# Optimization experiments

Measured on AMD Instinct MI355X. Metric: run time of the kernel, lower is better.

The kernel has to match this reference:

```python
import jax, jax.numpy as jnp
import numpy as np

B, T, D = 64, 512, 1024

def setup_inputs() -> dict:
    key = jax.random.key(0)
    k1, k2, k3 = jax.random.split(key, 3)
    q1 = jax.random.normal(k1, (B, T, D), dtype=jnp.float32)
    q2 = jax.random.normal(k2, (B, T, D), dtype=jnp.float32)
    # original uses 'uniform' init; scale like a small uniform weight
    U = jax.random.uniform(k3, (D, D), dtype=jnp.float32, minval=-0.05, maxval=0.05)
    return {"q1": q1, "q2": q2, "U": U}

def reference(q1, q2, U):
    # bilinear scores: (q1 @ U) @ q2^T -> [B, T1, T2]
    att = jnp.einsum('btd,de,bse->bts', q1, U, q2)
    att = jax.nn.relu(att)
    w1_att = jax.nn.softmax(att, axis=1)  # softmax over q1 timesteps
    w2_att = jax.nn.softmax(att, axis=2)  # softmax over q2 timesteps
    # q1_align = w1_att^T @ q1 -> [B, T2, D]
    q1_align = jnp.einsum('bts,btd->bsd', w1_att, q1)
    # q2_align = w2_att @ q2 -> [B, T1, D]
    q2_align = jnp.einsum('bts,bsd->btd', w2_att, q2)
    return (q1_align, q2_align)
```

## Files before the change

kernel.cpp:

```cpp
#include <hip/hip_runtime.h>
#include <hip/hip_bf16.h>
#include <math.h>

#define B_DIM 64
#define T_DIM 512
#define D_DIM 1024
#define TT (T_DIM * T_DIM)
#define TD (T_DIM * D_DIM)

typedef _Float16 f16;
typedef f16 f16x4 __attribute__((ext_vector_type(4)));
typedef f16 f16x8 __attribute__((ext_vector_type(8)));
typedef float f32x4 __attribute__((ext_vector_type(4)));


__device__ __forceinline__ void gld_lds16(const void* g, void* l) {
    __builtin_amdgcn_global_load_lds(
        (const __attribute__((address_space(1))) void*)g,
        (__attribute__((address_space(3))) void*)l, 16, 0, 0);
}

#define SWZ(r) (((r) >> 1) & 3)

template <int EPI>
__global__ __launch_bounds__(512, 2) void k_mfma2(
        const f16* __restrict__ A, int lda,
        const f16* __restrict__ Bt, int ldb, int K,
        void* __restrict__ Cout, int ldc,
        const float2* __restrict__ scaleP,
        long batchA, long batchB, long batchC,
        float2* __restrict__ rowP, float2* __restrict__ colP, long pstr,
        const f16* __restrict__ A2, const f16* __restrict__ Bt2,
        void* __restrict__ Cout2, const float2* __restrict__ scaleP2, int zsplit) {
    __shared__ f16 LA[2][8192];
    __shared__ f16 LB[2][8192];

    const int tid = threadIdx.x;
    const int lane = tid & 63, w = tid >> 6;

    const int gX = gridDim.x, gY = gridDim.y;
    int nwg = gX * gY * gridDim.z;
    int o = blockIdx.x + gX * (blockIdx.y + gY * blockIdx.z);
    int q8 = nwg >> 3, r8 = nwg & 7, xcd = o & 7, idx = o >> 3;
    int fl = (xcd < r8 ? xcd * (q8 + 1) : r8 * (q8 + 1) + (xcd - r8) * q8) + idx;
    const int bx = fl % gX;
    int tmp = fl / gX;
    const int by = tmp % gY;
    const int bz = tmp / gY;

    const f16* Au = A; const f16* Bu = Bt;
    void* Cu = Cout; const float2* su = scaleP;
    int zb = bz;
    if constexpr (EPI == 2) {
        if (bz >= zsplit) {
            zb = bz - zsplit;
            Au = A2; Bu = Bt2; Cu = Cout2; su = scaleP2;
        }
    }

    const f16* Ab = Au + (long)zb * batchA + (long)(by * 256) * lda;
    const f16* Bb = Bu + (long)zb * batchB + (long)(bx * 256) * ldb;

    const int r0 = tid >> 2, s0 = (tid & 3) ^ SWZ(r0);
    const int r1 = (512 + tid) >> 2, s1 = ((512 + tid) & 3) ^ SWZ(r1);
    const long offA0 = (long)r0 * lda + s0 * 8;
    const long offA1 = (long)r1 * lda + s1 * 8;
    const long offB0 = (long)r0 * ldb + s0 * 8;
    const long offB1 = (long)r1 * ldb + s1 * 8;
    const int ldsOff0 = w * 512;
    const int ldsOff1 = 4096 + w * 512;

    const int g = lane >> 4;
    const int rA0 = (w & 1) * 128 + (lane & 15);
    const int rB0 = (w >> 1) * 64 + (lane & 15);

    f32x4 acc[8][4] = {};

    gld_lds16(Ab + offA0, &LA[0][ldsOff0]);
    gld_lds16(Ab + offA1, &LA[0][ldsOff1]);
    gld_lds16(Bb + offB0, &LB[0][ldsOff0]);
    gld_lds16(Bb + offB1, &LB[0][ldsOff1]);
    __syncthreads();

    const int NT = K >> 5;
    for (int t = 0; t < NT; ++t) {
        const int cur = t & 1;
        if (t + 1 < NT) {
            const long kt = (long)(t + 1) << 5;
            gld_lds16(Ab + offA0 + kt, &LA[cur ^ 1][ldsOff0]);
            gld_lds16(Ab + offA1 + kt, &LA[cur ^ 1][ldsOff1]);
            gld_lds16(Bb + offB0 + kt, &LB[cur ^ 1][ldsOff0]);
            gld_lds16(Bb + offB1 + kt, &LB[cur ^ 1][ldsOff1]);
        }
        f16x8 a[8], b[4];
#pragma unroll
        for (int m = 0; m < 8; ++m) {
            int r = rA0 + m * 16;
            a[m] = *(const f16x8*)(&LA[cur][r * 32 + ((g ^ SWZ(r)) << 3)]);
        }
#pragma unroll
        for (int n = 0; n < 4; ++n) {
            int r = rB0 + n * 16;
            b[n] = *(const f16x8*)(&LB[cur][r * 32 + ((g ^ SWZ(r)) << 3)]);
        }
#pragma unroll
        for (int m = 0; m < 8; ++m)
#pragma unroll
            for (int n = 0; n < 4; ++n)
                acc[m][n] = __builtin_amdgcn_mfma_f32_16x16x32_f16(a[m], b[n], acc[m][n], 0, 0, 0);
        __syncthreads();
    }

    const int row0 = by * 256 + (w & 1) * 128 + (lane >> 4) * 4;
    const int col0 = bx * 256 + (w >> 1) * 64 + (lane & 15);

    if constexpr (EPI == 0) {
        f16* C = (f16*)Cu;
#pragma unroll
        for (int m = 0; m < 8; ++m)
#pragma unroll
            for (int r = 0; r < 4; ++r) {
                long row = row0 + m * 16 + r;
#pragma unroll
                for (int n = 0; n < 4; ++n)
                    C[row * ldc + col0 + n * 16] = (f16)acc[m][n][r];
            }
    } else if constexpr (EPI == 1) {
#pragma unroll
        for (int m = 0; m < 8; ++m)
#pragma unroll
            for (int n = 0; n < 4; ++n)
#pragma unroll
                for (int r = 0; r < 4; ++r)
                    acc[m][n][r] = fmaxf(acc[m][n][r], 0.0f);
        float* C = (float*)Cu + (long)zb * batchC;
#pragma unroll
        for (int m = 0; m < 8; ++m)
#pragma unroll
            for (int r = 0; r < 4; ++r) {
                long row = row0 + m * 16 + r;
#pragma unroll
                for (int n = 0; n < 4; ++n)
                    C[row * ldc + col0 + n * 16] = acc[m][n][r];
            }
        float* redR = (float*)(&LA[0][0]);
        float* redC = redR + 2048;
        const int h = w & 1, cw = w >> 1;
#pragma unroll
        for (int m = 0; m < 8; ++m)
#pragma unroll
            for (int r = 0; r < 4; ++r) {
                float mx = fmaxf(fmaxf(acc[m][0][r], acc[m][1][r]),
                                 fmaxf(acc[m][2][r], acc[m][3][r]));
                mx = fmaxf(mx, __shfl_xor(mx, 1));
                mx = fmaxf(mx, __shfl_xor(mx, 2));
                mx = fmaxf(mx, __shfl_xor(mx, 4));
                mx = fmaxf(mx, __shfl_xor(mx, 8));
                float sm = __expf(acc[m][0][r] - mx) + __expf(acc[m][1][r] - mx)
                         + __expf(acc[m][2][r] - mx) + __expf(acc[m][3][r] - mx);
                sm += __shfl_xor(sm, 1);
                sm += __shfl_xor(sm, 2);
                sm += __shfl_xor(sm, 4);
                sm += __shfl_xor(sm, 8);
                if ((lane & 15) == 0) {
                    int lr = m * 16 + (lane >> 4) * 4 + r;
                    redR[((h * 128 + lr) * 4 + cw) * 2 + 0] = mx;
                    redR[((h * 128 + lr) * 4 + cw) * 2 + 1] = sm;
                }
            }
#pragma unroll
        for (int n = 0; n < 4; ++n) {
            float mx = acc[0][n][0];
#pragma unroll
            for (int m = 0; m < 8; ++m)
#pragma unroll
                for (int r = 0; r < 4; ++r) mx = fmaxf(mx, acc[m][n][r]);
            mx = fmaxf(mx, __shfl_xor(mx, 16));
            mx = fmaxf(mx, __shfl_xor(mx, 32));
            float sm = 0.f;
#pragma unroll
            for (int m = 0; m < 8; ++m)
#pragma unroll
                for (int r = 0; r < 4; ++r) sm += __expf(acc[m][n][r] - mx);
            sm += __shfl_xor(sm, 16);
            sm += __shfl_xor(sm, 32);
            if (lane < 16) {
                int c = cw * 64 + n * 16 + lane;
                redC[(h * 256 + c) * 2 + 0] = mx;
                redC[(h * 256 + c) * 2 + 1] = sm;
            }
        }
        __syncthreads();
        if (tid < 256) {
            float M = -1e30f, S = 0.f;
#pragma unroll
            for (int i = 0; i < 4; ++i) {
                float m_ = redR[(tid * 4 + i) * 2 + 0];
                float s_ = redR[(tid * 4 + i) * 2 + 1];
                float nm = fmaxf(M, m_);
                S = S * __expf(M - nm) + s_ * __expf(m_ - nm);
                M = nm;
            }
            rowP[(long)bx * pstr + (long)bz * 512 + by * 256 + tid] = make_float2(M, S);
        } else {
            int c = tid - 256;
            float m0_ = redC[c * 2 + 0], s0_ = redC[c * 2 + 1];
            float m1_ = redC[(256 + c) * 2 + 0], s1_ = redC[(256 + c) * 2 + 1];
            float M = fmaxf(m0_, m1_);
            float S = s0_ * __expf(m0_ - M) + s1_ * __expf(m1_ - M);
            colP[(long)by * pstr + (long)bz * 512 + bx * 256 + c] = make_float2(M, S);
        }
    } else {
        float* C = (float*)Cu + (long)zb * batchC;
        const float2* sp = su + (long)zb * 512;
#pragma unroll
        for (int m = 0; m < 8; ++m)
#pragma unroll
            for (int r = 0; r < 4; ++r) {
                long row = row0 + m * 16 + r;
                float2 pa = sp[row], pb = sp[pstr + row];
                float M = fmaxf(pa.x, pb.x);
                float S = pa.y * __expf(pa.x - M) + pb.y * __expf(pb.x - M);
                float inv = 1.0f / S;
#pragma unroll
                for (int n = 0; n < 4; ++n)
                    C[row * ldc + col0 + n * 16] = acc[m][n][r] * inv;
            }
    }
}

__global__ __launch_bounds__(256) void k_cast_both(const float* __restrict__ q1,
                                                   const float* __restrict__ q2,
                                                   f16* __restrict__ q1h, f16* __restrict__ q1ht,
                                                   f16* __restrict__ q2h, f16* __restrict__ q2ht) {
    __shared__ f16 tr[64][72];
    int zz = blockIdx.z;
    int b = zz & 63;
    const float* src = (zz < 64) ? q1 : q2;
    f16* dst  = (zz < 64) ? q1h : q2h;
    f16* dstT = (zz < 64) ? q1ht : q2ht;
    int d0 = blockIdx.x * 64, t0 = blockIdx.y * 64;
    const float* S = src + ((size_t)b * T_DIM + t0) * D_DIM + d0;
    f16* Dr = dst + ((size_t)b * T_DIM + t0) * D_DIM + d0;
    int tid = threadIdx.x;
    int rr = tid >> 4, cc = (tid & 15) * 4;
#pragma unroll
    for (int i = 0; i < 4; ++i) {
        int r = rr + i * 16;
        float4 v = *(const float4*)(S + (size_t)r * D_DIM + cc);
        f16x4 h = {(f16)v.x, (f16)v.y, (f16)v.z, (f16)v.w};
        *(f16x4*)(Dr + (size_t)r * D_DIM + cc) = h;
        tr[cc + 0][r] = h[0];
        tr[cc + 1][r] = h[1];
        tr[cc + 2][r] = h[2];
        tr[cc + 3][r] = h[3];
    }
    __syncthreads();
    f16* Dt = dstT + ((size_t)b * D_DIM + d0) * T_DIM + t0;
    int r2 = tid >> 3, c8 = (tid & 7) * 8;
#pragma unroll
    for (int i = 0; i < 2; ++i) {
        int d = r2 + i * 32;
        f16x8 vv = *(const f16x8*)(&tr[d][c8]);
        *(f16x8*)(Dt + (size_t)d * T_DIM + c8) = vv;
    }
}

__global__ __launch_bounds__(256) void k_castU(const float* __restrict__ U,
                                               f16* __restrict__ Uht) {
    __shared__ f16 tr[64][72];
    int n0 = blockIdx.x * 64, k0 = blockIdx.y * 64;
    int tid = threadIdx.x;
    int rr = tid >> 4, cc = (tid & 15) * 4;
#pragma unroll
    for (int i = 0; i < 4; ++i) {
        int r = rr + i * 16;
        float4 v = *(const float4*)(U + (size_t)(k0 + r) * D_DIM + n0 + cc);
        tr[cc + 0][r] = (f16)v.x;
        tr[cc + 1][r] = (f16)v.y;
        tr[cc + 2][r] = (f16)v.z;
        tr[cc + 3][r] = (f16)v.w;
    }
    __syncthreads();
    int r2 = tid >> 3, c8 = (tid & 7) * 8;
#pragma unroll
    for (int i = 0; i < 2; ++i) {
        int n = r2 + i * 32;
        f16x8 vv = *(const f16x8*)(&tr[n][c8]);
        *(f16x8*)(Uht + (size_t)(n0 + n) * D_DIM + k0 + c8) = vv;
    }
}

__global__ __launch_bounds__(256) void k_pconv(const float* __restrict__ att,
                                               const float2* __restrict__ rowP,
                                               const float2* __restrict__ colP, long pstr,
                                               f16* __restrict__ P2, f16* __restrict__ P1) {
    __shared__ f16 tr[64][72];
    __shared__ float rmS[64], cmS[64];
    int z = blockIdx.z;
    int t0 = blockIdx.y * 64, s0 = blockIdx.x * 64;
    int tid = threadIdx.x;
    if (tid < 64) {
        float2 a = rowP[(long)z * 512 + t0 + tid];
        float2 b = rowP[pstr + (long)z * 512 + t0 + tid];
        rmS[tid] = fmaxf(a.x, b.x);
    } else if (tid < 128) {
        int s = tid - 64;
        float2 a = colP[(long)z * 512 + s0 + s];
        float2 b = colP[pstr + (long)z * 512 + s0 + s];
        cmS[s] = fmaxf(a.x, b.x);
    }
    __syncthreads();
    const float* S = att + (size_t)z * TT + (size_t)t0 * T_DIM + s0;
    int rr = tid >> 4, cc = (tid & 15) * 4;
#pragma unroll
    for (int i = 0; i < 4; ++i) {
        int r = rr + i * 16;
        float4 v = *(const float4*)(S + (size_t)r * T_DIM + cc);
        float m = rmS[r];
        f16x4 p2 = {(f16)__expf(v.x - m), (f16)__expf(v.y - m),
                    (f16)__expf(v.z - m), (f16)__expf(v.w - m)};
        *(f16x4*)(P2 + (size_t)z * TT + (size_t)(t0 + r) * T_DIM + s0 + cc) = p2;
        tr[cc + 0][r] = (f16)__expf(v.x - cmS[cc + 0]);
        tr[cc + 1][r] = (f16)__expf(v.y - cmS[cc + 1]);
        tr[cc + 2][r] = (f16)__expf(v.z - cmS[cc + 2]);
        tr[cc + 3][r] = (f16)__expf(v.w - cmS[cc + 3]);
    }
    __syncthreads();
    int r2 = tid >> 3, c8 = (tid & 7) * 8;
#pragma unroll
    for (int i = 0; i < 2; ++i) {
        int s = r2 + i * 32;
        f16x8 vv = *(const f16x8*)(&tr[s][c8]);
        *(f16x8*)(P1 + (size_t)z * TT + (size_t)(s0 + s) * T_DIM + t0 + c8) = vv;
    }
}

__global__ __launch_bounds__(256) void k_rowstats(const float* __restrict__ att,
                                                  float* __restrict__ rmax,
                                                  float* __restrict__ rsum, int b0) {
    int wave = threadIdx.x >> 6, lane = threadIdx.x & 63;
    int lr = blockIdx.x * 4 + wave;
    const float4* row = reinterpret_cast<const float4*>(att + (size_t)lr * T_DIM);
    float4 v0 = row[lane];
    float4 v1 = row[lane + 64];
    float m = fmaxf(fmaxf(fmaxf(v0.x, v0.y), fmaxf(v0.z, v0.w)),
                    fmaxf(fmaxf(v1.x, v1.y), fmaxf(v1.z, v1.w)));
#pragma unroll
    for (int off = 32; off >= 1; off >>= 1) m = fmaxf(m, __shfl_xor(m, off));
    float s = __expf(v0.x - m) + __expf(v0.y - m) + __expf(v0.z - m) + __expf(v0.w - m)
            + __expf(v1.x - m) + __expf(v1.y - m) + __expf(v1.z - m) + __expf(v1.w - m);
#pragma unroll
    for (int off = 32; off >= 1; off >>= 1) s += __shfl_xor(s, off);
    if (lane == 0) {
        size_t gr = (size_t)b0 * T_DIM + lr;
        rmax[gr] = m;
        rsum[gr] = s;
    }
}

__global__ __launch_bounds__(256) void k_colstats(const float* __restrict__ att,
                                                  float* __restrict__ cmax,
                                                  float* __restrict__ csum, int b0) {
    int lb = blockIdx.y;
    int s = blockIdx.x * 256 + threadIdx.x;
    const float* base = att + (size_t)lb * TT + s;
    float m = -INFINITY, sum = 0.f;
    for (int t = 0; t < T_DIM; ++t) {
        float x = base[(size_t)t * T_DIM];
        float nm = fmaxf(m, x);
        sum = sum * __expf(m - nm) + __expf(x - nm);
        m = nm;
    }
    size_t g = (size_t)(b0 + lb) * T_DIM + s;
    cmax[g] = m;
    csum[g] = sum;
}

#define BM 128
#define BN 128
#define BKK 16
#define APITCH 132

__device__ __forceinline__ void stage_a_rowmajor(float* As, const float* __restrict__ A,
                                                 int lda, int tid) {
#pragma unroll
    for (int i = 0; i < 2; ++i) {
        int idx = tid + i * 256;
        int r = idx >> 2;
        int k4 = (idx & 3) << 2;
        float4 v = *reinterpret_cast<const float4*>(&A[(size_t)r * lda + k4]);
        As[(k4 + 0) * APITCH + r] = v.x;
        As[(k4 + 1) * APITCH + r] = v.y;
        As[(k4 + 2) * APITCH + r] = v.z;
        As[(k4 + 3) * APITCH + r] = v.w;
    }
}
__device__ __forceinline__ void stage_a_rowmajor_exp(float* As, const float* __restrict__ A,
                                                     int lda, const float* __restrict__ rowmax,
                                                     int tid) {
#pragma unroll
    for (int i = 0; i < 2; ++i) {
        int idx = tid + i * 256;
        int r = idx >> 2;
        int k4 = (idx & 3) << 2;
        float4 v = *reinterpret_cast<const float4*>(&A[(size_t)r * lda + k4]);
        float m = rowmax[r];
        As[(k4 + 0) * APITCH + r] = __expf(v.x - m);
        As[(k4 + 1) * APITCH + r] = __expf(v.y - m);
        As[(k4 + 2) * APITCH + r] = __expf(v.z - m);
        As[(k4 + 3) * APITCH + r] = __expf(v.w - m);
    }
}
__device__ __forceinline__ void stage_a_colmajor_exp(float* As, const float* __restrict__ S,
                                                     int lds, const float* __restrict__ colmax,
                                                     int tid) {
#pragma unroll
    for (int i = 0; i < 2; ++i) {
        int idx = tid + i * 256;
        int k = idx >> 5;
        int m4 = (idx & 31) << 2;
        float4 v = *reinterpret_cast<const float4*>(&S[(size_t)k * lds + m4]);
        float4 c = *reinterpret_cast<const float4*>(&colmax[m4]);
        float4 o;
        o.x = __expf(v.x - c.x); o.y = __expf(v.y - c.y);
        o.z = __expf(v.z - c.z); o.w = __expf(v.w - c.w);
        *reinterpret_cast<float4*>(&As[k * APITCH + m4]) = o;
    }
}
__device__ __forceinline__ void stage_b_rowmajor(float* Bs, const float* __restrict__ Bp,
                                                 int ldb, int tid) {
#pragma unroll
    for (int i = 0; i < 2; ++i) {
        int idx = tid + i * 256;
        int k = idx >> 5;
        int c4 = idx & 31;
        float4 v = *reinterpret_cast<const float4*>(&Bp[(size_t)k * ldb + (c4 << 2)]);
        *reinterpret_cast<float4*>(&Bs[k * BN + ((c4 & 1) << 6) + ((c4 >> 1) << 2)]) = v;
    }
}
__device__ __forceinline__ void stage_b_transpose(float* Bs, const float* __restrict__ Q,
                                                  int ldq, int tid) {
#pragma unroll
    for (int i = 0; i < 2; ++i) {
        int idx = tid + i * 256;
        int s = idx >> 2;
        int e4 = (idx & 3) << 2;
        float4 v = *reinterpret_cast<const float4*>(&Q[(size_t)s * ldq + e4]);
        int sw = ((s & 4) << 4) + ((s >> 3) << 2) + (s & 3);
        Bs[(e4 + 0) * BN + sw] = v.x;
        Bs[(e4 + 1) * BN + sw] = v.y;
        Bs[(e4 + 2) * BN + sw] = v.z;
        Bs[(e4 + 3) * BN + sw] = v.w;
    }
}
__device__ __forceinline__ void gemm_inner(const float* As, const float* Bs,
                                           float acc[8][8], int tx, int ty) {
#pragma unroll
    for (int k = 0; k < BKK; ++k) {
        float4 a0 = *reinterpret_cast<const float4*>(&As[k * APITCH + ty * 8]);
        float4 a1 = *reinterpret_cast<const float4*>(&As[k * APITCH + ty * 8 + 4]);
        float4 b0 = *reinterpret_cast<const float4*>(&Bs[k * BN + tx * 4]);
        float4 b1 = *reinterpret_cast<const float4*>(&Bs[k * BN + 64 + tx * 4]);
        float a[8] = {a0.x, a0.y, a0.z, a0.w, a1.x, a1.y, a1.z, a1.w};
        float b[8] = {b0.x, b0.y, b0.z, b0.w, b1.x, b1.y, b1.z, b1.w};
#pragma unroll
        for (int i = 0; i < 8; ++i)
#pragma unroll
            for (int j = 0; j < 8; ++j)
                acc[i][j] = fmaf(a[i], b[j], acc[i][j]);
    }
}
__global__ __launch_bounds__(256) void k_gemm_qU(const float* __restrict__ q1,
                                                 const float* __restrict__ U,
                                                 float* __restrict__ qU, int b0) {
    __shared__ float As[BKK * APITCH];
    __shared__ float Bs[BKK * BN];
    int tid = threadIdx.x, tx = tid & 15, ty = tid >> 4;
    int m0 = blockIdx.y * BM;
    int n0 = blockIdx.x * BN;
    const float* Abase = q1 + (size_t)b0 * TD + (size_t)m0 * D_DIM;
    const float* Bbase = U + n0;
    float acc[8][8] = {};
    for (int kt = 0; kt < D_DIM; kt += BKK) {
        stage_a_rowmajor(As, Abase + kt, D_DIM, tid);
        stage_b_rowmajor(Bs, Bbase + (size_t)kt * D_DIM, D_DIM, tid);
        __syncthreads();
        gemm_inner(As, Bs, acc, tx, ty);
        __syncthreads();
    }
    float* Cp = qU + (size_t)m0 * D_DIM + n0;
#pragma unroll
    for (int i = 0; i < 8; ++i) {
        int r = ty * 8 + i;
        float4 o0 = {acc[i][0], acc[i][1], acc[i][2], acc[i][3]};
        float4 o1 = {acc[i][4], acc[i][5], acc[i][6], acc[i][7]};
        *reinterpret_cast<float4*>(&Cp[(size_t)r * D_DIM + tx * 8]) = o0;
        *reinterpret_cast<float4*>(&Cp[(size_t)r * D_DIM + tx * 8 + 4]) = o1;
    }
}
__global__ __launch_bounds__(256) void k_att(const float* __restrict__ qU,
                                             const float* __restrict__ q2,
                                             float* __restrict__ att, int b0) {
    __shared__ float As[BKK * APITCH];
    __shared__ float Bs[BKK * BN];
    int tid = threadIdx.x, tx = tid & 15, ty = tid >> 4;
    int lb = blockIdx.z;
    int m0 = blockIdx.y * BM;
    int n0 = blockIdx.x * BN;
    const float* Abase = qU + (size_t)lb * TD + (size_t)m0 * D_DIM;
    const float* Qbase = q2 + (size_t)(b0 + lb) * TD + (size_t)n0 * D_DIM;
    float acc[8][8] = {};
    for (int kt = 0; kt < D_DIM; kt += BKK) {
        stage_a_rowmajor(As, Abase + kt, D_DIM, tid);
        stage_b_transpose(Bs, Qbase + kt, D_DIM, tid);
        __syncthreads();
        gemm_inner(As, Bs, acc, tx, ty);
        __syncthreads();
    }
    float* Cp = att + (size_t)lb * TT + (size_t)m0 * T_DIM + n0;
#pragma unroll
    for (int i = 0; i < 8; ++i) {
        int r = ty * 8 + i;
        float4 o0 = {fmaxf(acc[i][0], 0.f), fmaxf(acc[i][1], 0.f), fmaxf(acc[i][2], 0.f), fmaxf(acc[i][3], 0.f)};
        float4 o1 = {fmaxf(acc[i][4], 0.f), fmaxf(acc[i][5], 0.f), fmaxf(acc[i][6], 0.f), fmaxf(acc[i][7], 0.f)};
        *reinterpret_cast<float4*>(&Cp[(size_t)r * T_DIM + tx * 8]) = o0;
        *reinterpret_cast<float4*>(&Cp[(size_t)r * T_DIM + tx * 8 + 4]) = o1;
    }
}
__global__ __launch_bounds__(256) void k_q2align(const float* __restrict__ att,
                                                 const float* __restrict__ q2,
                                                 const float* __restrict__ rmax,
                                                 const float* __restrict__ rsum,
                                                 float* __restrict__ out, int b0) {
    __shared__ float As[BKK * APITCH];
    __shared__ float Bs[BKK * BN];
    int tid = threadIdx.x, tx = tid & 15, ty = tid >> 4;
    int lb = blockIdx.z;
    int m0 = blockIdx.y * BM;
    int n0 = blockIdx.x * BN;
    const float* Abase = att + (size_t)lb * TT + (size_t)m0 * T_DIM;
    const float* rmaxp = rmax + (size_t)(b0 + lb) * T_DIM + m0;
    const float* rsump = rsum + (size_t)(b0 + lb) * T_DIM + m0;
    const float* Bbase = q2 + (size_t)(b0 + lb) * TD + n0;
    float acc[8][8] = {};
    for (int kt = 0; kt < T_DIM; kt += BKK) {
        stage_a_rowmajor_exp(As, Abase + kt, T_DIM, rmaxp, tid);
        stage_b_rowmajor(Bs, Bbase + (size_t)kt * D_DIM, D_DIM, tid);
        __syncthreads();
        gemm_inner(As, Bs, acc, tx, ty);
        __syncthreads();
    }
    float* Cp = out + (size_t)B_DIM * TD + (size_t)(b0 + lb) * TD + (size_t)m0 * D_DIM + n0;
#pragma unroll
    for (int i = 0; i < 8; ++i) {
        int r = ty * 8 + i;
        float inv = 1.0f / rsump[r];
        float4 o0 = {acc[i][0] * inv, acc[i][1] * inv, acc[i][2] * inv, acc[i][3] * inv};
        float4 o1 = {acc[i][4] * inv, acc[i][5] * inv, acc[i][6] * inv, acc[i][7] * inv};
        *reinterpret_cast<float4*>(&Cp[(size_t)r * D_DIM + tx * 8]) = o0;
        *reinterpret_cast<float4*>(&Cp[(size_t)r * D_DIM + tx * 8 + 4]) = o1;
    }
}
__global__ __launch_bounds__(256) void k_q1align(const float* __restrict__ att,
                                                 const float* __restrict__ q1,
                                                 const float* __restrict__ cmax,
                                                 const float* __restrict__ csum,
                                                 float* __restrict__ out, int b0) {
    __shared__ float As[BKK * APITCH];
    __shared__ float Bs[BKK * BN];
    int tid = threadIdx.x, tx = tid & 15, ty = tid >> 4;
    int lb = blockIdx.z;
    int m0 = blockIdx.y * BM;
    int n0 = blockIdx.x * BN;
    const float* Sbase = att + (size_t)lb * TT + m0;
    const float* cmaxp = cmax + (size_t)(b0 + lb) * T_DIM + m0;
    const float* csump = csum + (size_t)(b0 + lb) * T_DIM + m0;
    const float* Bbase = q1 + (size_t)(b0 + lb) * TD + n0;
    float acc[8][8] = {};
    for (int kt = 0; kt < T_DIM; kt += BKK) {
        stage_a_colmajor_exp(As, Sbase + (size_t)kt * T_DIM, T_DIM, cmaxp, tid);
        stage_b_rowmajor(Bs, Bbase + (size_t)kt * D_DIM, D_DIM, tid);
        __syncthreads();
        gemm_inner(As, Bs, acc, tx, ty);
        __syncthreads();
    }
    float* Cp = out + (size_t)(b0 + lb) * TD + (size_t)m0 * D_DIM + n0;
#pragma unroll
    for (int i = 0; i < 8; ++i) {
        int r = ty * 8 + i;
        float inv = 1.0f / csump[r];
        float4 o0 = {acc[i][0] * inv, acc[i][1] * inv, acc[i][2] * inv, acc[i][3] * inv};
        float4 o1 = {acc[i][4] * inv, acc[i][5] * inv, acc[i][6] * inv, acc[i][7] * inv};
        *reinterpret_cast<float4*>(&Cp[(size_t)r * D_DIM + tx * 8]) = o0;
        *reinterpret_cast<float4*>(&Cp[(size_t)r * D_DIM + tx * 8 + 4]) = o1;
    }
}

extern "C" void kernel_launch(void* const* d_in, const int* in_sizes, int n_in,
                              void* d_out, int out_size, void* d_ws, size_t ws_size,
                              hipStream_t stream) {
    const float* q1 = (const float*)d_in[0];
    const float* q2 = (const float*)d_in[1];
    const float* U  = (const float*)d_in[2];
    float* out = (float*)d_out;

    const size_t BT  = (size_t)B_DIM * T_DIM;
    const size_t BTD = (size_t)B_DIM * TD;
    const size_t DD  = (size_t)D_DIM * D_DIM;

    const size_t fixedB = (4 * BTD + DD) * 2;
    const size_t perbB  = (size_t)TD * 2 + (size_t)TT * 4 + (size_t)TT * 4
                        + 4ull * T_DIM * sizeof(float2);
    int C = 64;
    while (C > 1 && fixedB + (size_t)C * perbB > ws_size) C >>= 1;

    if (fixedB + perbB <= ws_size) {
        f16* q1h  = (f16*)d_ws;
        f16* q1ht = q1h  + BTD;
        f16* q2h  = q1ht + BTD;
        f16* q2ht = q2h  + BTD;
        f16* Uht  = q2ht + BTD;
        f16* qUh  = Uht  + DD;
        float* att = (float*)(qUh + (size_t)C * TD);
        f16* P2h  = (f16*)(att + (size_t)C * TT);
        f16* P1h  = P2h + (size_t)C * TT;
        float2* rowP = (float2*)(P1h + (size_t)C * TT);
        float2* colP = rowP + 2ull * C * T_DIM;
        const long pstr = (long)C * T_DIM;

        k_cast_both<<<dim3(16, 8, 128), 256, 0, stream>>>(q1, q2, q1h, q1ht, q2h, q2ht);
        k_castU<<<dim3(16, 16), 256, 0, stream>>>(U, Uht);

        for (int b0 = 0; b0 < B_DIM; b0 += C) {
            k_mfma2<0><<<dim3(4, C * 2, 1), 512, 0, stream>>>(
                q1h + (size_t)b0 * TD, D_DIM, Uht, D_DIM, D_DIM,
                qUh, D_DIM, nullptr, 0, 0, 0,
                nullptr, nullptr, 0, nullptr, nullptr, nullptr, nullptr, 0);
            k_mfma2<1><<<dim3(2, 2, C), 512, 0, stream>>>(
                qUh, D_DIM, q2h + (size_t)b0 * TD, D_DIM, D_DIM,
                att, T_DIM, nullptr, (long)TD, (long)TD, (long)TT,
                rowP, colP, pstr, nullptr, nullptr, nullptr, nullptr, 0);
            k_pconv<<<dim3(8, 8, C), 256, 0, stream>>>(att, rowP, colP, pstr, P2h, P1h);
            k_mfma2<2><<<dim3(4, 2, 2 * C), 512, 0, stream>>>(
                P2h, T_DIM, q2ht + (size_t)b0 * TD, T_DIM, T_DIM,
                out + BTD + (size_t)b0 * TD, D_DIM, rowP,
                (long)TT, (long)TD, (long)TD,
                nullptr, nullptr, pstr,
                P1h, q1ht + (size_t)b0 * TD,
                out + (size_t)b0 * TD, colP, C);
        }
        return;
    }

    const size_t statsElems = 4ull * B_DIM * T_DIM;
    float* rmax = (float*)d_ws;
    float* rsum = rmax + BT;
    float* cmax = rsum + BT;
    float* csum = cmax + BT;
    float* scratch = csum + BT;
    size_t availFloats = (ws_size > statsElems * 4) ? (ws_size - statsElems * 4) / 4 : 0;
    int C2 = 64;
    while (C2 > 1 && (size_t)C2 * (TD + TT) > availFloats) C2 >>= 1;
    if ((size_t)C2 * (TD + TT) > availFloats) return;
    float* qU  = scratch;
    float* att = qU + (size_t)C2 * TD;
    for (int b0 = 0; b0 < B_DIM; b0 += C2) {
        k_gemm_qU<<<dim3(D_DIM / BN, C2 * (T_DIM / BM)), 256, 0, stream>>>(q1, U, qU, b0);
        k_att<<<dim3(T_DIM / BN, T_DIM / BM, C2), 256, 0, stream>>>(qU, q2, att, b0);
        k_rowstats<<<dim3(C2 * T_DIM / 4), 256, 0, stream>>>(att, rmax, rsum, b0);
        k_colstats<<<dim3(T_DIM / 256, C2), 256, 0, stream>>>(att, cmax, csum, b0);
        k_q2align<<<dim3(D_DIM / BN, T_DIM / BM, C2), 256, 0, stream>>>(att, q2, rmax, rsum, out, b0);
        k_q1align<<<dim3(D_DIM / BN, T_DIM / BM, C2), 256, 0, stream>>>(att, q1, cmax, csum, out, b0);
    }
}
```

Measured before the change: 452.5 us.

## Fuse casts into GEMM launches and compute row-softmax probabilities inside align GEMM

```diff
diff --git a/kernel.cpp b/kernel.cpp
--- a/kernel.cpp
+++ b/kernel.cpp
@@ -7,12 +7,12 @@
 #define D_DIM 1024
 #define TT (T_DIM * T_DIM)
 #define TD (T_DIM * D_DIM)
+#define PSTR ((long)B_DIM * T_DIM)
 
 typedef _Float16 f16;
 typedef f16 f16x4 __attribute__((ext_vector_type(4)));
 typedef f16 f16x8 __attribute__((ext_vector_type(8)));
 typedef float f32x4 __attribute__((ext_vector_type(4)));
-
 
 __device__ __forceinline__ void gld_lds16(const void* g, void* l) {
     __builtin_amdgcn_global_load_lds(
@@ -29,11 +29,9 @@
         void* __restrict__ Cout, int ldc,
         const float2* __restrict__ scaleP,
         long batchA, long batchB, long batchC,
-        float2* __restrict__ rowP, float2* __restrict__ colP, long pstr,
-        const f16* __restrict__ A2, const f16* __restrict__ Bt2,
-        void* __restrict__ Cout2, const float2* __restrict__ scaleP2, int zsplit) {
-    __shared__ f16 LA[2][8192];
-    __shared__ f16 LB[2][8192];
+        float2* __restrict__ rowP, float2* __restrict__ colP) {
+    __shared__ __align__(16) f16 LA[2][8192];
+    __shared__ __align__(16) f16 LB[2][8192];
 
     const int tid = threadIdx.x;
     const int lane = tid & 63, w = tid >> 6;
@@ -41,28 +39,18 @@
     const int gX = gridDim.x, gY = gridDim.y;
     int nwg = gX * gY * gridDim.z;
     int o = blockIdx.x + gX * (blockIdx.y + gY * blockIdx.z);
-    int q8 = nwg >> 3, r8 = nwg & 7, xcd = o & 7, idx = o >> 3;
-    int fl = (xcd < r8 ? xcd * (q8 + 1) : r8 * (q8 + 1) + (xcd - r8) * q8) + idx;
+    int q8 = nwg >> 3;
+    int fl = (o & 7) * q8 + (o >> 3);
     const int bx = fl % gX;
     int tmp = fl / gX;
     const int by = tmp % gY;
     const int bz = tmp / gY;
 
-    const f16* Au = A; const f16* Bu = Bt;
-    void* Cu = Cout; const float2* su = scaleP;
-    int zb = bz;
-    if constexpr (EPI == 2) {
-        if (bz >= zsplit) {
-            zb = bz - zsplit;
-            Au = A2; Bu = Bt2; Cu = Cout2; su = scaleP2;
-        }
-    }
-
-    const f16* Ab = Au + (long)zb * batchA + (long)(by * 256) * lda;
-    const f16* Bb = Bu + (long)zb * batchB + (long)(bx * 256) * ldb;
+    const f16* Ab = A + (long)bz * batchA + (long)(by * 256) * lda;
+    const f16* Bb = Bt + (long)bz * batchB + (long)(bx * 256) * ldb;
 
     const int r0 = tid >> 2, s0 = (tid & 3) ^ SWZ(r0);
-    const int r1 = (512 + tid) >> 2, s1 = ((512 + tid) & 3) ^ SWZ(r1);
+    const int r1 = r0 + 128, s1 = (tid & 3) ^ SWZ(r1);
     const long offA0 = (long)r0 * lda + s0 * 8;
     const long offA1 = (long)r1 * lda + s1 * 8;
     const long offB0 = (long)r0 * ldb + s0 * 8;
@@ -103,29 +91,20 @@
             int r = rB0 + n * 16;
             b[n] = *(const f16x8*)(&LB[cur][r * 32 + ((g ^ SWZ(r)) << 3)]);
         }
+        __builtin_amdgcn_s_setprio(1);
 #pragma unroll
         for (int m = 0; m < 8; ++m)
 #pragma unroll
             for (int n = 0; n < 4; ++n)
                 acc[m][n] = __builtin_amdgcn_mfma_f32_16x16x32_f16(a[m], b[n], acc[m][n], 0, 0, 0);
+        __builtin_amdgcn_s_setprio(0);
         __syncthreads();
     }
 
     const int row0 = by * 256 + (w & 1) * 128 + (lane >> 4) * 4;
     const int col0 = bx * 256 + (w >> 1) * 64 + (lane & 15);
 
-    if constexpr (EPI == 0) {
-        f16* C = (f16*)Cu;
-#pragma unroll
-        for (int m = 0; m < 8; ++m)
-#pragma unroll
-            for (int r = 0; r < 4; ++r) {
-                long row = row0 + m * 16 + r;
-#pragma unroll
-                for (int n = 0; n < 4; ++n)
-                    C[row * ldc + col0 + n * 16] = (f16)acc[m][n][r];
-            }
-    } else if constexpr (EPI == 1) {
+    if constexpr (EPI == 1) {
 #pragma unroll
         for (int m = 0; m < 8; ++m)
 #pragma unroll
@@ -133,7 +112,7 @@
 #pragma unroll
                 for (int r = 0; r < 4; ++r)
                     acc[m][n][r] = fmaxf(acc[m][n][r], 0.0f);
-        float* C = (float*)Cu + (long)zb * batchC;
+        float* C = (float*)Cout + (long)bz * batchC;
 #pragma unroll
         for (int m = 0; m < 8; ++m)
 #pragma unroll
@@ -201,24 +180,24 @@
                 S = S * __expf(M - nm) + s_ * __expf(m_ - nm);
                 M = nm;
             }
-            rowP[(long)bx * pstr + (long)bz * 512 + by * 256 + tid] = make_float2(M, S);
+            rowP[(long)bx * PSTR + (long)bz * 512 + by * 256 + tid] = make_float2(M, S);
         } else {
             int c = tid - 256;
             float m0_ = redC[c * 2 + 0], s0_ = redC[c * 2 + 1];
             float m1_ = redC[(256 + c) * 2 + 0], s1_ = redC[(256 + c) * 2 + 1];
             float M = fmaxf(m0_, m1_);
             float S = s0_ * __expf(m0_ - M) + s1_ * __expf(m1_ - M);
-            colP[(long)by * pstr + (long)bz * 512 + bx * 256 + c] = make_float2(M, S);
+            colP[(long)by * PSTR + (long)bz * 512 + bx * 256 + c] = make_float2(M, S);
         }
     } else {
-        float* C = (float*)Cu + (long)zb * batchC;
-        const float2* sp = su + (long)zb * 512;
+        float* C = (float*)Cout + (long)bz * batchC;
+        const float2* sp = scaleP + (long)bz * 512;
 #pragma unroll
         for (int m = 0; m < 8; ++m)
 #pragma unroll
             for (int r = 0; r < 4; ++r) {
                 long row = row0 + m * 16 + r;
-                float2 pa = sp[row], pb = sp[pstr + row];
+                float2 pa = sp[row], pb = sp[PSTR + row];
                 float M = fmaxf(pa.x, pb.x);
                 float S = pa.y * __expf(pa.x - M) + pb.y * __expf(pb.x - M);
                 float inv = 1.0f / S;
@@ -229,371 +208,330 @@
     }
 }
 
-__global__ __launch_bounds__(256) void k_cast_both(const float* __restrict__ q1,
-                                                   const float* __restrict__ q2,
-                                                   f16* __restrict__ q1h, f16* __restrict__ q1ht,
-                                                   f16* __restrict__ q2h, f16* __restrict__ q2ht) {
+__global__ __launch_bounds__(256) void k_d1(const float* __restrict__ q1,
+                                            f16* __restrict__ q1h, f16* __restrict__ q1ht,
+                                            const float* __restrict__ U,
+                                            f16* __restrict__ Uht) {
     __shared__ f16 tr[64][72];
-    int zz = blockIdx.z;
-    int b = zz & 63;
-    const float* src = (zz < 64) ? q1 : q2;
-    f16* dst  = (zz < 64) ? q1h : q2h;
-    f16* dstT = (zz < 64) ? q1ht : q2ht;
-    int d0 = blockIdx.x * 64, t0 = blockIdx.y * 64;
-    const float* S = src + ((size_t)b * T_DIM + t0) * D_DIM + d0;
-    f16* Dr = dst + ((size_t)b * T_DIM + t0) * D_DIM + d0;
     int tid = threadIdx.x;
-    int rr = tid >> 4, cc = (tid & 15) * 4;
-#pragma unroll
-    for (int i = 0; i < 4; ++i) {
-        int r = rr + i * 16;
-        float4 v = *(const float4*)(S + (size_t)r * D_DIM + cc);
-        f16x4 h = {(f16)v.x, (f16)v.y, (f16)v.z, (f16)v.w};
-        *(f16x4*)(Dr + (size_t)r * D_DIM + cc) = h;
-        tr[cc + 0][r] = h[0];
-        tr[cc + 1][r] = h[1];
-        tr[cc + 2][r] = h[2];
-        tr[cc + 3][r] = h[3];
-    }
-    __syncthreads();
-    f16* Dt = dstT + ((size_t)b * D_DIM + d0) * T_DIM + t0;
-    int r2 = tid >> 3, c8 = (tid & 7) * 8;
-#pragma unroll
-    for (int i = 0; i < 2; ++i) {
-        int d = r2 + i * 32;
-        f16x8 vv = *(const f16x8*)(&tr[d][c8]);
-        *(f16x8*)(Dt + (size_t)d * T_DIM + c8) = vv;
+    int z = blockIdx.z;
+    if (z < 64) {
+        int b = z;
+        int d0 = blockIdx.x * 64, t0 = blockIdx.y * 64;
+        const float* S = q1 + ((size_t)b * T_DIM + t0) * D_DIM + d0;
+        f16* Dr = q1h + ((size_t)b * T_DIM + t0) * D_DIM + d0;
+        int rr = tid >> 4, cc = (tid & 15) * 4;
+#pragma unroll
+        for (int i = 0; i < 4; ++i) {
+            int r = rr + i * 16;
+            float4 v = *(const float4*)(S + (size_t)r * D_DIM + cc);
+            f16x4 h = {(f16)v.x, (f16)v.y, (f16)v.z, (f16)v.w};
+            *(f16x4*)(Dr + (size_t)r * D_DIM + cc) = h;
+            tr[cc + 0][r] = h[0];
+            tr[cc + 1][r] = h[1];
+            tr[cc + 2][r] = h[2];
+            tr[cc + 3][r] = h[3];
+        }
+        __syncthreads();
+        f16* Dt = q1ht + ((size_t)b * D_DIM + d0) * T_DIM + t0;
+        int r2 = tid >> 3, c8 = (tid & 7) * 8;
+#pragma unroll
+        for (int i = 0; i < 2; ++i) {
+            int d = r2 + i * 32;
+            f16x8 vv = *(const f16x8*)(&tr[d][c8]);
+            *(f16x8*)(Dt + (size_t)d * T_DIM + c8) = vv;
+        }
+    } else {
+        int pos = blockIdx.y * 16 + blockIdx.x;
+        for (int u = 0; u < 2; ++u) {
+            int tile = pos + u * 128;
+            int n0 = (tile & 15) * 64, k0 = (tile >> 4) * 64;
+            int rr = tid >> 4, cc = (tid & 15) * 4;
+#pragma unroll
+            for (int i = 0; i < 4; ++i) {
+                int r = rr + i * 16;
+                float4 v = *(const float4*)(U + (size_t)(k0 + r) * D_DIM + n0 + cc);
+                tr[cc + 0][r] = (f16)v.x;
+                tr[cc + 1][r] = (f16)v.y;
+                tr[cc + 2][r] = (f16)v.z;
+                tr[cc + 3][r] = (f16)v.w;
+            }
+            __syncthreads();
+            int r2 = tid >> 3, c8 = (tid & 7) * 8;
+#pragma unroll
+            for (int i = 0; i < 2; ++i) {
+                int n = r2 + i * 32;
+                f16x8 vv = *(const f16x8*)(&tr[n][c8]);
+                *(f16x8*)(Uht + (size_t)(n0 + n) * D_DIM + k0 + c8) = vv;
+            }
+            __syncthreads();
+        }
     }
 }
 
-__global__ __launch_bounds__(256) void k_castU(const float* __restrict__ U,
-                                               f16* __restrict__ Uht) {
-    __shared__ f16 tr[64][72];
-    int n0 = blockIdx.x * 64, k0 = blockIdx.y * 64;
+__global__ __launch_bounds__(512, 2) void k_d2(const f16* __restrict__ q1h,
+                                               const f16* __restrict__ Uht,
+                                               f16* __restrict__ qUh,
+                                               const float* __restrict__ q2,
+                                               f16* __restrict__ q2h,
+                                               f16* __restrict__ q2ht) {
+    __shared__ __align__(16) f16 SM[32768];
     int tid = threadIdx.x;
-    int rr = tid >> 4, cc = (tid & 15) * 4;
-#pragma unroll
-    for (int i = 0; i < 4; ++i) {
-        int r = rr + i * 16;
-        float4 v = *(const float4*)(U + (size_t)(k0 + r) * D_DIM + n0 + cc);
-        tr[cc + 0][r] = (f16)v.x;
-        tr[cc + 1][r] = (f16)v.y;
-        tr[cc + 2][r] = (f16)v.z;
-        tr[cc + 3][r] = (f16)v.w;
-    }
-    __syncthreads();
-    int r2 = tid >> 3, c8 = (tid & 7) * 8;
-#pragma unroll
-    for (int i = 0; i < 2; ++i) {
-        int n = r2 + i * 32;
-        f16x8 vv = *(const f16x8*)(&tr[n][c8]);
-        *(f16x8*)(Uht + (size_t)(n0 + n) * D_DIM + k0 + c8) = vv;
+    if (blockIdx.y < 128) {
+        f16 (*LA)[8192] = (f16(*)[8192])SM;
+        f16 (*LB)[8192] = (f16(*)[8192])(SM + 16384);
+        const int lane = tid & 63, w = tid >> 6;
+        int o = blockIdx.x + 4 * blockIdx.y;
+        int fl = (o & 7) * 64 + (o >> 3);
+        int bx = fl & 3, by = fl >> 2;
+        const f16* Ab = q1h + (long)(by * 256) * D_DIM;
+        const f16* Bb = Uht + (long)(bx * 256) * D_DIM;
+
+        const int r0 = tid >> 2, s0 = (tid & 3) ^ SWZ(r0);
+        const int r1 = r0 + 128, s1 = (tid & 3) ^ SWZ(r1);
+        const long offA0 = (long)r0 * D_DIM + s0 * 8;
+        const long offA1 = (long)r1 * D_DIM + s1 * 8;
+        const int ldsOff0 = w * 512, ldsOff1 = 4096 + w * 512;
+        const int g = lane >> 4;
+        const int rA0 = (w & 1) * 128 + (lane & 15);
+        const int rB0 = (w >> 1) * 64 + (lane & 15);
+
+        f32x4 acc[8][4] = {};
+        gld_lds16(Ab + offA0, &LA[0][ldsOff0]);
+        gld_lds16(Ab + offA1, &LA[0][ldsOff1]);
+        gld_lds16(Bb + offA0, &LB[0][ldsOff0]);
+        gld_lds16(Bb + offA1, &LB[0][ldsOff1]);
+        __syncthreads();
+
+        for (int t = 0; t < 32; ++t) {
+            const int cur = t & 1;
+            if (t + 1 < 32) {
+                const long kt = (long)(t + 1) << 5;
+                gld_lds16(Ab + offA0 + kt, &LA[cur ^ 1][ldsOff0]);
+                gld_lds16(Ab + offA1 + kt, &LA[cur ^ 1][ldsOff1]);
+                gld_lds16(Bb + offA0 + kt, &LB[cur ^ 1][ldsOff0]);
+                gld_lds16(Bb + offA1 + kt, &LB[cur ^ 1][ldsOff1]);
+            }
+            f16x8 a[8], b[4];
+#pragma unroll
+            for (int m = 0; m < 8; ++m) {
+                int r = rA0 + m * 16;
+                a[m] = *(const f16x8*)(&LA[cur][r * 32 + ((g ^ SWZ(r)) << 3)]);
+            }
+#pragma unroll
+            for (int n = 0; n < 4; ++n) {
+                int r = rB0 + n * 16;
+                b[n] = *(const f16x8*)(&LB[cur][r * 32 + ((g ^ SWZ(r)) << 3)]);
+            }
+            __builtin_amdgcn_s_setprio(1);
+#pragma unroll
+            for (int m = 0; m < 8; ++m)
+#pragma unroll
+                for (int n = 0; n < 4; ++n)
+                    acc[m][n] = __builtin_amdgcn_mfma_f32_16x16x32_f16(a[m], b[n], acc[m][n], 0, 0, 0);
+            __builtin_amdgcn_s_setprio(0);
+            __syncthreads();
+        }
+        const int row0 = by * 256 + (w & 1) * 128 + (lane >> 4) * 4;
+        const int col0 = bx * 256 + (w >> 1) * 64 + (lane & 15);
+#pragma unroll
+        for (int m = 0; m < 8; ++m)
+#pragma unroll
+            for (int r = 0; r < 4; ++r) {
+                long row = row0 + m * 16 + r;
+#pragma unroll
+                for (int n = 0; n < 4; ++n)
+                    qUh[row * D_DIM + col0 + n * 16] = (f16)acc[m][n][r];
+            }
+    } else {
+        int hf = tid >> 8, t2 = tid & 255;
+        f16 (*tr)[72] = (f16(*)[72])(SM + hf * 4608);
+        int p = (blockIdx.y - 128) * 4 + blockIdx.x;
+        int tile = p * 2 + hf;
+        int b = tile >> 7, rem = tile & 127;
+        int d0 = (rem & 15) * 64, t0 = (rem >> 4) * 64;
+        const float* S = q2 + ((size_t)b * T_DIM + t0) * D_DIM + d0;
+        f16* Dr = q2h + ((size_t)b * T_DIM + t0) * D_DIM + d0;
+        int rr = t2 >> 4, cc = (t2 & 15) * 4;
+#pragma unroll
+        for (int i = 0; i < 4; ++i) {
+            int r = rr + i * 16;
+            float4 v = *(const float4*)(S + (size_t)r * D_DIM + cc);
+            f16x4 h = {(f16)v.x, (f16)v.y, (f16)v.z, (f16)v.w};
+            *(f16x4*)(Dr + (size_t)r * D_DIM + cc) = h;
+            tr[cc + 0][r] = h[0];
+            tr[cc + 1][r] = h[1];
+            tr[cc + 2][r] = h[2];
+            tr[cc + 3][r] = h[3];
+        }
+        __syncthreads();
+        f16* Dt = q2ht + ((size_t)b * D_DIM + d0) * T_DIM + t0;
+        int r2 = t2 >> 3, c8 = (t2 & 7) * 8;
+#pragma unroll
+        for (int i = 0; i < 2; ++i) {
+            int d = r2 + i * 32;
+            f16x8 vv = *(const f16x8*)(&tr[d][c8]);
+            *(f16x8*)(Dt + (size_t)d * T_DIM + c8) = vv;
+        }
     }
 }
 
-__global__ __launch_bounds__(256) void k_pconv(const float* __restrict__ att,
+__global__ __launch_bounds__(512, 2) void k_d4(const float* __restrict__ att,
+                                               const f16* __restrict__ q2ht,
                                                const float2* __restrict__ rowP,
-                                               const float2* __restrict__ colP, long pstr,
-                                               f16* __restrict__ P2, f16* __restrict__ P1) {
-    __shared__ f16 tr[64][72];
-    __shared__ float rmS[64], cmS[64];
+                                               const float2* __restrict__ colP,
+                                               float* __restrict__ out2,
+                                               f16* __restrict__ P1h) {
+    __shared__ __align__(16) f16 SM[33280];
+    int tid = threadIdx.x;
     int z = blockIdx.z;
-    int t0 = blockIdx.y * 64, s0 = blockIdx.x * 64;
-    int tid = threadIdx.x;
-    if (tid < 64) {
-        float2 a = rowP[(long)z * 512 + t0 + tid];
-        float2 b = rowP[pstr + (long)z * 512 + t0 + tid];
-        rmS[tid] = fmaxf(a.x, b.x);
-    } else if (tid < 128) {
-        int s = tid - 64;
-        float2 a = colP[(long)z * 512 + s0 + s];
-        float2 b = colP[pstr + (long)z * 512 + s0 + s];
-        cmS[s] = fmaxf(a.x, b.x);
-    }
-    __syncthreads();
-    const float* S = att + (size_t)z * TT + (size_t)t0 * T_DIM + s0;
-    int rr = tid >> 4, cc = (tid & 15) * 4;
-#pragma unroll
-    for (int i = 0; i < 4; ++i) {
-        int r = rr + i * 16;
-        float4 v = *(const float4*)(S + (size_t)r * T_DIM + cc);
-        float m = rmS[r];
-        f16x4 p2 = {(f16)__expf(v.x - m), (f16)__expf(v.y - m),
-                    (f16)__expf(v.z - m), (f16)__expf(v.w - m)};
-        *(f16x4*)(P2 + (size_t)z * TT + (size_t)(t0 + r) * T_DIM + s0 + cc) = p2;
-        tr[cc + 0][r] = (f16)__expf(v.x - cmS[cc + 0]);
-        tr[cc + 1][r] = (f16)__expf(v.y - cmS[cc + 1]);
-        tr[cc + 2][r] = (f16)__expf(v.z - cmS[cc + 2]);
-        tr[cc + 3][r] = (f16)__expf(v.w - cmS[cc + 3]);
-    }
-    __syncthreads();
-    int r2 = tid >> 3, c8 = (tid & 7) * 8;
-#pragma unroll
-    for (int i = 0; i < 2; ++i) {
-        int s = r2 + i * 32;
-        f16x8 vv = *(const f16x8*)(&tr[s][c8]);
-        *(f16x8*)(P1 + (size_t)z * TT + (size_t)(s0 + s) * T_DIM + t0 + c8) = vv;
-    }
-}
-
-__global__ __launch_bounds__(256) void k_rowstats(const float* __restrict__ att,
-                                                  float* __restrict__ rmax,
-                                                  float* __restrict__ rsum, int b0) {
-    int wave = threadIdx.x >> 6, lane = threadIdx.x & 63;
-    int lr = blockIdx.x * 4 + wave;
-    const float4* row = reinterpret_cast<const float4*>(att + (size_t)lr * T_DIM);
-    float4 v0 = row[lane];
-    float4 v1 = row[lane + 64];
-    float m = fmaxf(fmaxf(fmaxf(v0.x, v0.y), fmaxf(v0.z, v0.w)),
-                    fmaxf(fmaxf(v1.x, v1.y), fmaxf(v1.z, v1.w)));
-#pragma unroll
-    for (int off = 32; off >= 1; off >>= 1) m = fmaxf(m, __shfl_xor(m, off));
-    float s = __expf(v0.x - m) + __expf(v0.y - m) + __expf(v0.z - m) + __expf(v0.w - m)
-            + __expf(v1.x - m) + __expf(v1.y - m) + __expf(v1.z - m) + __expf(v1.w - m);
-#pragma unroll
-    for (int off = 32; off >= 1; off >>= 1) s += __shfl_xor(s, off);
-    if (lane == 0) {
-        size_t gr = (size_t)b0 * T_DIM + lr;
-        rmax[gr] = m;
-        rsum[gr] = s;
-    }
-}
-
-__global__ __launch_bounds__(256) void k_colstats(const float* __restrict__ att,
-                                                  float* __restrict__ cmax,
-                                                  float* __restrict__ csum, int b0) {
-    int lb = blockIdx.y;
-    int s = blockIdx.x * 256 + threadIdx.x;
-    const float* base = att + (size_t)lb * TT + s;
-    float m = -INFINITY, sum = 0.f;
-    for (int t = 0; t < T_DIM; ++t) {
-        float x = base[(size_t)t * T_DIM];
-        float nm = fmaxf(m, x);
-        sum = sum * __expf(m - nm) + __expf(x - nm);
-        m = nm;
-    }
-    size_t g = (size_t)(b0 + lb) * T_DIM + s;
-    cmax[g] = m;
-    csum[g] = sum;
-}
-
-#define BM 128
-#define BN 128
-#define BKK 16
-#define APITCH 132
-
-__device__ __forceinline__ void stage_a_rowmajor(float* As, const float* __restrict__ A,
-                                                 int lda, int tid) {
-#pragma unroll
-    for (int i = 0; i < 2; ++i) {
-        int idx = tid + i * 256;
-        int r = idx >> 2;
-        int k4 = (idx & 3) << 2;
-        float4 v = *reinterpret_cast<const float4*>(&A[(size_t)r * lda + k4]);
-        As[(k4 + 0) * APITCH + r] = v.x;
-        As[(k4 + 1) * APITCH + r] = v.y;
-        As[(k4 + 2) * APITCH + r] = v.z;
-        As[(k4 + 3) * APITCH + r] = v.w;
-    }
-}
-__device__ __forceinline__ void stage_a_rowmajor_exp(float* As, const float* __restrict__ A,
-                                                     int lda, const float* __restrict__ rowmax,
-                                                     int tid) {
-#pragma unroll
-    for (int i = 0; i < 2; ++i) {
-        int idx = tid + i * 256;
-        int r = idx >> 2;
-        int k4 = (idx & 3) << 2;
-        float4 v = *reinterpret_cast<const float4*>(&A[(size_t)r * lda + k4]);
-        float m = rowmax[r];
-        As[(k4 + 0) * APITCH + r] = __expf(v.x - m);
-        As[(k4 + 1) * APITCH + r] = __expf(v.y - m);
-        As[(k4 + 2) * APITCH + r] = __expf(v.z - m);
-        As[(k4 + 3) * APITCH + r] = __expf(v.w - m);
-    }
-}
-__device__ __forceinline__ void stage_a_colmajor_exp(float* As, const float* __restrict__ S,
-                                                     int lds, const float* __restrict__ colmax,
-                                                     int tid) {
-#pragma unroll
-    for (int i = 0; i < 2; ++i) {
-        int idx = tid + i * 256;
-        int k = idx >> 5;
-        int m4 = (idx & 31) << 2;
-        float4 v = *reinterpret_cast<const float4*>(&S[(size_t)k * lds + m4]);
-        float4 c = *reinterpret_cast<const float4*>(&colmax[m4]);
-        float4 o;
-        o.x = __expf(v.x - c.x); o.y = __expf(v.y - c.y);
-        o.z = __expf(v.z - c.z); o.w = __expf(v.w - c.w);
-        *reinterpret_cast<float4*>(&As[k * APITCH + m4]) = o;
-    }
-}
-__device__ __forceinline__ void stage_b_rowmajor(float* Bs, const float* __restrict__ Bp,
-                                                 int ldb, int tid) {
-#pragma unroll
-    for (int i = 0; i < 2; ++i) {
-        int idx = tid + i * 256;
-        int k = idx >> 5;
-        int c4 = idx & 31;
-        float4 v = *reinterpret_cast<const float4*>(&Bp[(size_t)k * ldb + (c4 << 2)]);
-        *reinterpret_cast<float4*>(&Bs[k * BN + ((c4 & 1) << 6) + ((c4 >> 1) << 2)]) = v;
-    }
-}
-__device__ __forceinline__ void stage_b_transpose(float* Bs, const float* __restrict__ Q,
-                                                  int ldq, int tid) {
-#pragma unroll
-    for (int i = 0; i < 2; ++i) {
-        int idx = tid + i * 256;
-        int s = idx >> 2;
-        int e4 = (idx & 3) << 2;
-        float4 v = *reinterpret_cast<const float4*>(&Q[(size_t)s * ldq + e4]);
-        int sw = ((s & 4) << 4) + ((s >> 3) << 2) + (s & 3);
-        Bs[(e4 + 0) * BN + sw] = v.x;
-        Bs[(e4 + 1) * BN + sw] = v.y;
-        Bs[(e4 + 2) * BN + sw] = v.z;
-        Bs[(e4 + 3) * BN + sw] = v.w;
-    }
-}
-__device__ __forceinline__ void gemm_inner(const float* As, const float* Bs,
-                                           float acc[8][8], int tx, int ty) {
-#pragma unroll
-    for (int k = 0; k < BKK; ++k) {
-        float4 a0 = *reinterpret_cast<const float4*>(&As[k * APITCH + ty * 8]);
-        float4 a1 = *reinterpret_cast<const float4*>(&As[k * APITCH + ty * 8 + 4]);
-        float4 b0 = *reinterpret_cast<const float4*>(&Bs[k * BN + tx * 4]);
-        float4 b1 = *reinterpret_cast<const float4*>(&Bs[k * BN + 64 + tx * 4]);
-        float a[8] = {a0.x, a0.y, a0.z, a0.w, a1.x, a1.y, a1.z, a1.w};
-        float b[8] = {b0.x, b0.y, b0.z, b0.w, b1.x, b1.y, b1.z, b1.w};
-#pragma unroll
-        for (int i = 0; i < 8; ++i)
-#pragma unroll
-            for (int j = 0; j < 8; ++j)
-                acc[i][j] = fmaf(a[i], b[j], acc[i][j]);
-    }
-}
-__global__ __launch_bounds__(256) void k_gemm_qU(const float* __restrict__ q1,
-                                                 const float* __restrict__ U,
-                                                 float* __restrict__ qU, int b0) {
-    __shared__ float As[BKK * APITCH];
-    __shared__ float Bs[BKK * BN];
-    int tid = threadIdx.x, tx = tid & 15, ty = tid >> 4;
-    int m0 = blockIdx.y * BM;
-    int n0 = blockIdx.x * BN;
-    const float* Abase = q1 + (size_t)b0 * TD + (size_t)m0 * D_DIM;
-    const float* Bbase = U + n0;
-    float acc[8][8] = {};
-    for (int kt = 0; kt < D_DIM; kt += BKK) {
-        stage_a_rowmajor(As, Abase + kt, D_DIM, tid);
-        stage_b_rowmajor(Bs, Bbase + (size_t)kt * D_DIM, D_DIM, tid);
-        __syncthreads();
-        gemm_inner(As, Bs, acc, tx, ty);
-        __syncthreads();
-    }
-    float* Cp = qU + (size_t)m0 * D_DIM + n0;
-#pragma unroll
-    for (int i = 0; i < 8; ++i) {
-        int r = ty * 8 + i;
-        float4 o0 = {acc[i][0], acc[i][1], acc[i][2], acc[i][3]};
-        float4 o1 = {acc[i][4], acc[i][5], acc[i][6], acc[i][7]};
-        *reinterpret_cast<float4*>(&Cp[(size_t)r * D_DIM + tx * 8]) = o0;
-        *reinterpret_cast<float4*>(&Cp[(size_t)r * D_DIM + tx * 8 + 4]) = o1;
-    }
-}
-__global__ __launch_bounds__(256) void k_att(const float* __restrict__ qU,
-                                             const float* __restrict__ q2,
-                                             float* __restrict__ att, int b0) {
-    __shared__ float As[BKK * APITCH];
-    __shared__ float Bs[BKK * BN];
-    int tid = threadIdx.x, tx = tid & 15, ty = tid >> 4;
-    int lb = blockIdx.z;
-    int m0 = blockIdx.y * BM;
-    int n0 = blockIdx.x * BN;
-    const float* Abase = qU + (size_t)lb * TD + (size_t)m0 * D_DIM;
-    const float* Qbase = q2 + (size_t)(b0 + lb) * TD + (size_t)n0 * D_DIM;
-    float acc[8][8] = {};
-    for (int kt = 0; kt < D_DIM; kt += BKK) {
-        stage_a_rowmajor(As, Abase + kt, D_DIM, tid);
-        stage_b_transpose(Bs, Qbase + kt, D_DIM, tid);
-        __syncthreads();
-        gemm_inner(As, Bs, acc, tx, ty);
-        __syncthreads();
-    }
-    float* Cp = att + (size_t)lb * TT + (size_t)m0 * T_DIM + n0;
-#pragma unroll
-    for (int i = 0; i < 8; ++i) {
-        int r = ty * 8 + i;
-        float4 o0 = {fmaxf(acc[i][0], 0.f), fmaxf(acc[i][1], 0.f), fmaxf(acc[i][2], 0.f), fmaxf(acc[i][3], 0.f)};
-        float4 o1 = {fmaxf(acc[i][4], 0.f), fmaxf(acc[i][5], 0.f), fmaxf(acc[i][6], 0.f), fmaxf(acc[i][7], 0.f)};
-        *reinterpret_cast<float4*>(&Cp[(size_t)r * T_DIM + tx * 8]) = o0;
-        *reinterpret_cast<float4*>(&Cp[(size_t)r * T_DIM + tx * 8 + 4]) = o1;
-    }
-}
-__global__ __launch_bounds__(256) void k_q2align(const float* __restrict__ att,
-                                                 const float* __restrict__ q2,
-                                                 const float* __restrict__ rmax,
-                                                 const float* __restrict__ rsum,
-                                                 float* __restrict__ out, int b0) {
-    __shared__ float As[BKK * APITCH];
-    __shared__ float Bs[BKK * BN];
-    int tid = threadIdx.x, tx = tid & 15, ty = tid >> 4;
-    int lb = blockIdx.z;
-    int m0 = blockIdx.y * BM;
-    int n0 = blockIdx.x * BN;
-    const float* Abase = att + (size_t)lb * TT + (size_t)m0 * T_DIM;
-    const float* rmaxp = rmax + (size_t)(b0 + lb) * T_DIM + m0;
-    const float* rsump = rsum + (size_t)(b0 + lb) * T_DIM + m0;
-    const float* Bbase = q2 + (size_t)(b0 + lb) * TD + n0;
-    float acc[8][8] = {};
-    for (int kt = 0; kt < T_DIM; kt += BKK) {
-        stage_a_rowmajor_exp(As, Abase + kt, T_DIM, rmaxp, tid);
-        stage_b_rowmajor(Bs, Bbase + (size_t)kt * D_DIM, D_DIM, tid);
-        __syncthreads();
-        gemm_inner(As, Bs, acc, tx, ty);
-        __syncthreads();
-    }
-    float* Cp = out + (size_t)B_DIM * TD + (size_t)(b0 + lb) * TD + (size_t)m0 * D_DIM + n0;
-#pragma unroll
-    for (int i = 0; i < 8; ++i) {
-        int r = ty * 8 + i;
-        float inv = 1.0f / rsump[r];
-        float4 o0 = {acc[i][0] * inv, acc[i][1] * inv, acc[i][2] * inv, acc[i][3] * inv};
-        float4 o1 = {acc[i][4] * inv, acc[i][5] * inv, acc[i][6] * inv, acc[i][7] * inv};
-        *reinterpret_cast<float4*>(&Cp[(size_t)r * D_DIM + tx * 8]) = o0;
-        *reinterpret_cast<float4*>(&Cp[(size_t)r * D_DIM + tx * 8 + 4]) = o1;
-    }
-}
-__global__ __launch_bounds__(256) void k_q1align(const float* __restrict__ att,
-                                                 const float* __restrict__ q1,
-                                                 const float* __restrict__ cmax,
-                                                 const float* __restrict__ csum,
-                                                 float* __restrict__ out, int b0) {
-    __shared__ float As[BKK * APITCH];
-    __shared__ float Bs[BKK * BN];
-    int tid = threadIdx.x, tx = tid & 15, ty = tid >> 4;
-    int lb = blockIdx.z;
-    int m0 = blockIdx.y * BM;
-    int n0 = blockIdx.x * BN;
-    const float* Sbase = att + (size_t)lb * TT + m0;
-    const float* cmaxp = cmax + (size_t)(b0 + lb) * T_DIM + m0;
-    const float* csump = csum + (size_t)(b0 + lb) * T_DIM + m0;
-    const float* Bbase = q1 + (size_t)(b0 + lb) * TD + n0;
-    float acc[8][8] = {};
-    for (int kt = 0; kt < T_DIM; kt += BKK) {
-        stage_a_colmajor_exp(As, Sbase + (size_t)kt * T_DIM, T_DIM, cmaxp, tid);
-        stage_b_rowmajor(Bs, Bbase + (size_t)kt * D_DIM, D_DIM, tid);
-        __syncthreads();
-        gemm_inner(As, Bs, acc, tx, ty);
-        __syncthreads();
-    }
-    float* Cp = out + (size_t)(b0 + lb) * TD + (size_t)m0 * D_DIM + n0;
-#pragma unroll
-    for (int i = 0; i < 8; ++i) {
-        int r = ty * 8 + i;
-        float inv = 1.0f / csump[r];
-        float4 o0 = {acc[i][0] * inv, acc[i][1] * inv, acc[i][2] * inv, acc[i][3] * inv};
-        float4 o1 = {acc[i][4] * inv, acc[i][5] * inv, acc[i][6] * inv, acc[i][7] * inv};
-        *reinterpret_cast<float4*>(&Cp[(size_t)r * D_DIM + tx * 8]) = o0;
-        *reinterpret_cast<float4*>(&Cp[(size_t)r * D_DIM + tx * 8 + 4]) = o1;
+    if (z < 64) {
+        f16 (*LA)[8192] = (f16(*)[8192])SM;
+        f16 (*LB)[8192] = (f16(*)[8192])(SM + 16384);
+        float* rmS = (float*)(SM + 32768);
+        const int lane = tid & 63, w = tid >> 6;
+        int o = blockIdx.x + 4 * blockIdx.y + 8 * z;
+        int fl = (o & 7) * 64 + (o >> 3);
+        int bx = fl & 3, by = (fl >> 2) & 1, zb = fl >> 3;
+
+        const float* Abase = att + (long)zb * TT + (long)(by * 256) * T_DIM;
+        const f16* Bb = q2ht + (long)zb * TD + (long)(bx * 256) * T_DIM;
+
+        if (tid < 256) {
+            float2 pa = rowP[(long)zb * 512 + by * 256 + tid];
+            float2 pb = rowP[PSTR + (long)zb * 512 + by * 256 + tid];
+            rmS[tid] = fmaxf(pa.x, pb.x);
+        }
+
+        const int r0 = tid >> 2, j0 = tid & 3;
+        const int r1 = r0 + 128;
+        const int sb0 = j0 ^ SWZ(r0), sb1 = j0 ^ SWZ(r1);
+        const long offB0 = (long)r0 * T_DIM + sb0 * 8;
+        const long offB1 = (long)r1 * T_DIM + sb1 * 8;
+        const int ldsOff0 = w * 512, ldsOff1 = 4096 + w * 512;
+        const int wA0 = r0 * 32 + ((j0 ^ SWZ(r0)) << 3);
+        const int wA1 = r1 * 32 + ((j0 ^ SWZ(r1)) << 3);
+        const long srcA0 = (long)r0 * T_DIM + j0 * 8;
+        const long srcA1 = (long)r1 * T_DIM + j0 * 8;
+
+        const int g = lane >> 4;
+        const int rA0 = (w & 1) * 128 + (lane & 15);
+        const int rB0 = (w >> 1) * 64 + (lane & 15);
+
+        __syncthreads();
+        const float m0 = rmS[r0], m1 = rmS[r1];
+
+        f32x4 acc[8][4] = {};
+        {
+            float4 v0 = *(const float4*)(Abase + srcA0);
+            float4 v1 = *(const float4*)(Abase + srcA0 + 4);
+            float4 v2 = *(const float4*)(Abase + srcA1);
+            float4 v3 = *(const float4*)(Abase + srcA1 + 4);
+            f16x8 h0 = {(f16)__expf(v0.x - m0), (f16)__expf(v0.y - m0),
+                        (f16)__expf(v0.z - m0), (f16)__expf(v0.w - m0),
+                        (f16)__expf(v1.x - m0), (f16)__expf(v1.y - m0),
+                        (f16)__expf(v1.z - m0), (f16)__expf(v1.w - m0)};
+            f16x8 h1 = {(f16)__expf(v2.x - m1), (f16)__expf(v2.y - m1),
+                        (f16)__expf(v2.z - m1), (f16)__expf(v2.w - m1),
+                        (f16)__expf(v3.x - m1), (f16)__expf(v3.y - m1),
+                        (f16)__expf(v3.z - m1), (f16)__expf(v3.w - m1)};
+            *(f16x8*)(&LA[0][wA0]) = h0;
+            *(f16x8*)(&LA[0][wA1]) = h1;
+            gld_lds16(Bb + offB0, &LB[0][ldsOff0]);
+            gld_lds16(Bb + offB1, &LB[0][ldsOff1]);
+        }
+        __syncthreads();
+
+        for (int t = 0; t < 16; ++t) {
+            const int cur = t & 1;
+            float4 v0, v1, v2, v3;
+            if (t + 1 < 16) {
+                const long kc = (long)(t + 1) << 5;
+                v0 = *(const float4*)(Abase + srcA0 + kc);
+                v1 = *(const float4*)(Abase + srcA0 + kc + 4);
+                v2 = *(const float4*)(Abase + srcA1 + kc);
+                v3 = *(const float4*)(Abase + srcA1 + kc + 4);
+                gld_lds16(Bb + offB0 + kc, &LB[cur ^ 1][ldsOff0]);
+                gld_lds16(Bb + offB1 + kc, &LB[cur ^ 1][ldsOff1]);
+            }
+            f16x8 a[8], b[4];
+#pragma unroll
+            for (int m = 0; m < 8; ++m) {
+                int r = rA0 + m * 16;
+                a[m] = *(const f16x8*)(&LA[cur][r * 32 + ((g ^ SWZ(r)) << 3)]);
+            }
+#pragma unroll
+            for (int n = 0; n < 4; ++n) {
+                int r = rB0 + n * 16;
+                b[n] = *(const f16x8*)(&LB[cur][r * 32 + ((g ^ SWZ(r)) << 3)]);
+            }
+            __builtin_amdgcn_s_setprio(1);
+#pragma unroll
+            for (int m = 0; m < 8; ++m)
+#pragma unroll
+                for (int n = 0; n < 4; ++n)
+                    acc[m][n] = __builtin_amdgcn_mfma_f32_16x16x32_f16(a[m], b[n], acc[m][n], 0, 0, 0);
+            __builtin_amdgcn_s_setprio(0);
+            if (t + 1 < 16) {
+                f16x8 h0 = {(f16)__expf(v0.x - m0), (f16)__expf(v0.y - m0),
+                            (f16)__expf(v0.z - m0), (f16)__expf(v0.w - m0),
+                            (f16)__expf(v1.x - m0), (f16)__expf(v1.y - m0),
+                            (f16)__expf(v1.z - m0), (f16)__expf(v1.w - m0)};
+                f16x8 h1 = {(f16)__expf(v2.x - m1), (f16)__expf(v2.y - m1),
+                            (f16)__expf(v2.z - m1), (f16)__expf(v2.w - m1),
+                            (f16)__expf(v3.x - m1), (f16)__expf(v3.y - m1),
+                            (f16)__expf(v3.z - m1), (f16)__expf(v3.w - m1)};
+                *(f16x8*)(&LA[cur ^ 1][wA0]) = h0;
+                *(f16x8*)(&LA[cur ^ 1][wA1]) = h1;
+            }
+            __syncthreads();
+        }
+
+        const int row0 = by * 256 + (w & 1) * 128 + (lane >> 4) * 4;
+        const int col0 = bx * 256 + (w >> 1) * 64 + (lane & 15);
+        float* C = out2 + (long)zb * TD;
+        const float2* sp = rowP + (long)zb * 512;
+#pragma unroll
+        for (int m = 0; m < 8; ++m)
+#pragma unroll
+            for (int r = 0; r < 4; ++r) {
+                long row = row0 + m * 16 + r;
+                float2 pa = sp[row], pb = sp[PSTR + row];
+                float M = fmaxf(pa.x, pb.x);
+                float S = pa.y * __expf(pa.x - M) + pb.y * __expf(pb.x - M);
+                float inv = 1.0f / S;
+#pragma unroll
+                for (int n = 0; n < 4; ++n)
+                    C[row * D_DIM + col0 + n * 16] = acc[m][n][r] * inv;
+            }
+    } else {
+        f16 (*tr)[72] = (f16(*)[72])SM;
+        float* cmS = (float*)(SM + 16384);
+        int id = (z - 64) * 8 + blockIdx.y * 4 + blockIdx.x;
+        int b = id >> 6, rem = id & 63;
+        int t0 = (rem >> 3) * 64, s0 = (rem & 7) * 64;
+        if (tid < 64) {
+            float2 pa = colP[(long)b * 512 + s0 + tid];
+            float2 pb = colP[PSTR + (long)b * 512 + s0 + tid];
+            cmS[tid] = fmaxf(pa.x, pb.x);
+        }
+        __syncthreads();
+        const float* S = att + (long)b * TT + (long)t0 * T_DIM + s0;
+        int rr = tid >> 4, cc = (tid & 15) * 4;
+#pragma unroll
+        for (int i = 0; i < 2; ++i) {
+            int r = rr + i * 32;
+            float4 v = *(const float4*)(S + (long)r * T_DIM + cc);
+            tr[cc + 0][r] = (f16)__expf(v.x - cmS[cc + 0]);
+            tr[cc + 1][r] = (f16)__expf(v.y - cmS[cc + 1]);
+            tr[cc + 2][r] = (f16)__expf(v.z - cmS[cc + 2]);
+            tr[cc + 3][r] = (f16)__expf(v.w - cmS[cc + 3]);
+        }
+        __syncthreads();
+        f16* Dt = P1h + (long)b * TT + (long)s0 * T_DIM + t0;
+        int r2 = tid >> 3, c8 = (tid & 7) * 8;
+        f16x8 vv = *(const f16x8*)(&tr[r2][c8]);
+        *(f16x8*)(Dt + (long)r2 * T_DIM + c8) = vv;
     }
 }
 
@@ -605,72 +543,35 @@
     const float* U  = (const float*)d_in[2];
     float* out = (float*)d_out;
 
-    const size_t BT  = (size_t)B_DIM * T_DIM;
     const size_t BTD = (size_t)B_DIM * TD;
     const size_t DD  = (size_t)D_DIM * D_DIM;
-
-    const size_t fixedB = (4 * BTD + DD) * 2;
-    const size_t perbB  = (size_t)TD * 2 + (size_t)TT * 4 + (size_t)TT * 4
-                        + 4ull * T_DIM * sizeof(float2);
-    int C = 64;
-    while (C > 1 && fixedB + (size_t)C * perbB > ws_size) C >>= 1;
-
-    if (fixedB + perbB <= ws_size) {
-        f16* q1h  = (f16*)d_ws;
-        f16* q1ht = q1h  + BTD;
-        f16* q2h  = q1ht + BTD;
-        f16* q2ht = q2h  + BTD;
-        f16* Uht  = q2ht + BTD;
-        f16* qUh  = Uht  + DD;
-        float* att = (float*)(qUh + (size_t)C * TD);
-        f16* P2h  = (f16*)(att + (size_t)C * TT);
-        f16* P1h  = P2h + (size_t)C * TT;
-        float2* rowP = (float2*)(P1h + (size_t)C * TT);
-        float2* colP = rowP + 2ull * C * T_DIM;
-        const long pstr = (long)C * T_DIM;
-
-        k_cast_both<<<dim3(16, 8, 128), 256, 0, stream>>>(q1, q2, q1h, q1ht, q2h, q2ht);
-        k_castU<<<dim3(16, 16), 256, 0, stream>>>(U, Uht);
-
-        for (int b0 = 0; b0 < B_DIM; b0 += C) {
-            k_mfma2<0><<<dim3(4, C * 2, 1), 512, 0, stream>>>(
-                q1h + (size_t)b0 * TD, D_DIM, Uht, D_DIM, D_DIM,
-                qUh, D_DIM, nullptr, 0, 0, 0,
-                nullptr, nullptr, 0, nullptr, nullptr, nullptr, nullptr, 0);
-            k_mfma2<1><<<dim3(2, 2, C), 512, 0, stream>>>(
-                qUh, D_DIM, q2h + (size_t)b0 * TD, D_DIM, D_DIM,
-                att, T_DIM, nullptr, (long)TD, (long)TD, (long)TT,
-                rowP, colP, pstr, nullptr, nullptr, nullptr, nullptr, 0);
-            k_pconv<<<dim3(8, 8, C), 256, 0, stream>>>(att, rowP, colP, pstr, P2h, P1h);
-            k_mfma2<2><<<dim3(4, 2, 2 * C), 512, 0, stream>>>(
-                P2h, T_DIM, q2ht + (size_t)b0 * TD, T_DIM, T_DIM,
-                out + BTD + (size_t)b0 * TD, D_DIM, rowP,
-                (long)TT, (long)TD, (long)TD,
-                nullptr, nullptr, pstr,
-                P1h, q1ht + (size_t)b0 * TD,
-                out + (size_t)b0 * TD, colP, C);
-        }
-        return;
-    }
-
-    const size_t statsElems = 4ull * B_DIM * T_DIM;
-    float* rmax = (float*)d_ws;
-    float* rsum = rmax + BT;
-    float* cmax = rsum + BT;
-    float* csum = cmax + BT;
-    float* scratch = csum + BT;
-    size_t availFloats = (ws_size > statsElems * 4) ? (ws_size - statsElems * 4) / 4 : 0;
-    int C2 = 64;
-    while (C2 > 1 && (size_t)C2 * (TD + TT) > availFloats) C2 >>= 1;
-    if ((size_t)C2 * (TD + TT) > availFloats) return;
-    float* qU  = scratch;
-    float* att = qU + (size_t)C2 * TD;
-    for (int b0 = 0; b0 < B_DIM; b0 += C2) {
-        k_gemm_qU<<<dim3(D_DIM / BN, C2 * (T_DIM / BM)), 256, 0, stream>>>(q1, U, qU, b0);
-        k_att<<<dim3(T_DIM / BN, T_DIM / BM, C2), 256, 0, stream>>>(qU, q2, att, b0);
-        k_rowstats<<<dim3(C2 * T_DIM / 4), 256, 0, stream>>>(att, rmax, rsum, b0);
-        k_colstats<<<dim3(T_DIM / 256, C2), 256, 0, stream>>>(att, cmax, csum, b0);
-        k_q2align<<<dim3(D_DIM / BN, T_DIM / BM, C2), 256, 0, stream>>>(att, q2, rmax, rsum, out, b0);
-        k_q1align<<<dim3(D_DIM / BN, T_DIM / BM, C2), 256, 0, stream>>>(att, q1, cmax, csum, out, b0);
-    }
+    const size_t BTT = (size_t)B_DIM * TT;
+
+    const size_t need = (5 * BTD + DD) * 2
+                      + BTT * 4
+                      + BTT * 2
+                      + 4 * (size_t)PSTR * sizeof(float2);
+    if (need > ws_size) return;
+
+    f16* q1h  = (f16*)d_ws;
+    f16* q1ht = q1h  + BTD;
+    f16* q2h  = q1ht + BTD;
+    f16* q2ht = q2h  + BTD;
+    f16* Uht  = q2ht + BTD;
+    f16* qUh  = Uht  + DD;
+    float* att = (float*)(qUh + BTD);
+    f16* P1h  = (f16*)(att + BTT);
+    float2* rowP = (float2*)(P1h + BTT);
+    float2* colP = rowP + 2 * (size_t)PSTR;
+
+    k_d1<<<dim3(16, 8, 65), 256, 0, stream>>>(q1, q1h, q1ht, U, Uht);
+    k_d2<<<dim3(4, 128 + 1024, 1), 512, 0, stream>>>(q1h, Uht, qUh, q2, q2h, q2ht);
+    k_mfma2<1><<<dim3(2, 2, 64), 512, 0, stream>>>(
+        qUh, D_DIM, q2h, D_DIM, D_DIM, att, T_DIM,
+        nullptr, (long)TD, (long)TD, (long)TT, rowP, colP);
+    k_d4<<<dim3(4, 2, 64 + 512), 512, 0, stream>>>(
+        att, q2ht, rowP, colP, out + BTD, P1h);
+    k_mfma2<2><<<dim3(4, 2, 64), 512, 0, stream>>>(
+        P1h, T_DIM, q1ht, T_DIM, T_DIM, out, D_DIM,
+        colP, (long)TT, (long)TD, (long)TD, nullptr, nullptr);
 }
```

After: 422.0 us. 1.07x faster.
